# Optimization experiments

Hardware: AMD Instinct MI355X
Metric: run time of the kernel (lower is better)

## Reference

```python
import jax, jax.numpy as jnp
import numpy as np

NEG_SLOPE = 0.2


def setup_inputs() -> dict:
    key = jax.random.key(0)
    k1, k2, k3 = jax.random.split(key, 3)
    bs, n_agents, input_dim = 32, 512, 128
    n_heads, hidden_dim = 8, 64
    h = jax.random.normal(k1, (bs, n_agents, input_dim), dtype=jnp.float32)
    # Linear(input_dim, n_heads*hidden_dim, bias=False), stored as [in, out]
    W = jax.random.normal(k2, (input_dim, n_heads * hidden_dim), dtype=jnp.float32) * (1.0 / np.sqrt(input_dim))
    # xavier_uniform with gain=1.414 on shape (1, n_heads, 2*hidden_dim)
    fan = n_heads + 2 * hidden_dim
    bound = 1.414 * np.sqrt(6.0 / fan)
    att_a = jax.random.uniform(k3, (1, n_heads, 2 * hidden_dim), dtype=jnp.float32,
                               minval=-bound, maxval=bound)
    return {"h": h, "W": W, "att_a": att_a}


def reference(h, W, att_a):
    bs, n_agents, _ = h.shape
    n_heads = att_a.shape[1]
    hidden_dim = att_a.shape[2] // 2
    # h_prime: [bs, n_heads, n_agents, hidden_dim]
    h_prime = (h @ W).reshape(bs, n_agents, n_heads, hidden_dim).transpose(0, 2, 1, 3)
    # Additive score decomposes exactly: (a1.h_i + a2.h_j) == sum(cat(h_i,h_j)*a)
    a_src = att_a[0, :, :hidden_dim]   # [n_heads, hidden_dim]
    a_dst = att_a[0, :, hidden_dim:]   # [n_heads, hidden_dim]
    e_src = jnp.einsum('bhnd,hd->bhn', h_prime, a_src)  # score contribution of node i (row)
    e_dst = jnp.einsum('bhnd,hd->bhn', h_prime, a_dst)  # contribution of node j (col)
    e = e_src[:, :, :, None] + e_dst[:, :, None, :]     # [bs, n_heads, n, n]
    e = jnp.where(e >= 0, e, NEG_SLOPE * e)             # leaky_relu(0.2)
    attention = jax.nn.softmax(e, axis=-1)
    h_new = jnp.einsum('bhnm,bhmd->bhnd', attention, h_prime)
    return jax.nn.elu(h_new)
```

## Files before the change

kernel.cpp:

```cpp
#include <hip/hip_runtime.h>

#define BS 32
#define NA 512
#define ID 128
#define NH 8
#define HD 64
#define NHD 512
#define NEG 0.2f
#define BPAD 136
#define VSTR 520

typedef short bf16x8 __attribute__((ext_vector_type(8)));
typedef float f32x4 __attribute__((ext_vector_type(4)));
typedef int   i32x4 __attribute__((ext_vector_type(4)));

__device__ inline unsigned f2bf_bits(float x) {
  unsigned u = __float_as_uint(x);
  return (u + 0x7FFFu + ((u >> 16) & 1u)) >> 16;
}

__device__ inline void split8(const float4& x, const float4& y,
                              bf16x8& hi, bf16x8& lo) {
  float f[8] = {x.x, x.y, x.z, x.w, y.x, y.y, y.z, y.w};
  #pragma unroll
  for (int j = 0; j < 8; ++j) {
    unsigned hb = f2bf_bits(f[j]);
    float r = f[j] - __uint_as_float(hb << 16);
    unsigned lb = f2bf_bits(r);
    hi[j] = (short)hb;
    lo[j] = (short)lb;
  }
}

__global__ __launch_bounds__(256, 4) void k1_mfma(
    const float* __restrict__ h, const float* __restrict__ W,
    const float* __restrict__ att, float* __restrict__ hp,
    float* __restrict__ sG, float* __restrict__ tG) {
  __shared__ unsigned short Bhi[64 * BPAD];
  __shared__ unsigned short Blo[64 * BPAD];

  int blk = blockIdx.x;
  int mt = blk >> 3;
  int n0 = (blk & 7) * 64;
  int m0 = mt * 128;
  int b = mt >> 2;
  int nbase = (mt & 3) * 128;
  int head = n0 >> 6;
  int t = threadIdx.x;
  int lane = t & 63, w = t >> 6;
  int q = lane >> 4, ml = lane & 15;

  {
    int c = t & 63, kq = t >> 6;
    const float* wsrc = W + (size_t)kq * 32 * NHD + n0 + c;
    #pragma unroll 4
    for (int kk = 0; kk < 32; ++kk) {
      int k = kq * 32 + kk;
      float x = wsrc[(size_t)kk * NHD];
      unsigned hb = f2bf_bits(x);
      float r = x - __uint_as_float(hb << 16);
      Bhi[c * BPAD + k] = (unsigned short)hb;
      Blo[c * BPAD + k] = (unsigned short)f2bf_bits(r);
    }
  }
  __syncthreads();

  f32x4 acc[2][4];
  #pragma unroll
  for (int mf = 0; mf < 2; ++mf)
    #pragma unroll
    for (int nf = 0; nf < 4; ++nf)
      acc[mf][nf] = (f32x4){0.f, 0.f, 0.f, 0.f};

  const float* A0 = h + (size_t)(m0 + w * 32 + ml) * ID;

  #pragma unroll
  for (int ks = 0; ks < 4; ++ks) {
    int ko = ks * 32 + q * 8;
    bf16x8 ah[2], al[2];
    #pragma unroll
    for (int mf = 0; mf < 2; ++mf) {
      const float* ap = A0 + mf * 16 * ID + ko;
      float4 f0 = *(const float4*)ap;
      float4 f1 = *(const float4*)(ap + 4);
      split8(f0, f1, ah[mf], al[mf]);
    }
    #pragma unroll
    for (int nf = 0; nf < 4; ++nf) {
      int bo = (nf * 16 + ml) * BPAD + ko;
      bf16x8 bh = *(const bf16x8*)&Bhi[bo];
      bf16x8 bl = *(const bf16x8*)&Blo[bo];
      #pragma unroll
      for (int mf = 0; mf < 2; ++mf) {
        acc[mf][nf] = __builtin_amdgcn_mfma_f32_16x16x32_bf16(ah[mf], bh, acc[mf][nf], 0, 0, 0);
        acc[mf][nf] = __builtin_amdgcn_mfma_f32_16x16x32_bf16(ah[mf], bl, acc[mf][nf], 0, 0, 0);
        acc[mf][nf] = __builtin_amdgcn_mfma_f32_16x16x32_bf16(al[mf], bh, acc[mf][nf], 0, 0, 0);
      }
    }
  }

  {
    float* ob = hp + (((size_t)b * NH + head) * NA + nbase + w * 32) * HD + ml;
    #pragma unroll
    for (int mf = 0; mf < 2; ++mf)
      #pragma unroll
      for (int nf = 0; nf < 4; ++nf)
        #pragma unroll
        for (int r = 0; r < 4; ++r)
          ob[(size_t)(mf * 16 + q * 4 + r) * HD + nf * 16] = acc[mf][nf][r];
  }

  {
    float a_s[4], a_d[4];
    #pragma unroll
    for (int nf = 0; nf < 4; ++nf) {
      a_s[nf] = att[head * 128 + nf * 16 + ml];
      a_d[nf] = att[head * 128 + 64 + nf * 16 + ml];
    }
    #pragma unroll
    for (int mf = 0; mf < 2; ++mf) {
      #pragma unroll
      for (int r = 0; r < 4; ++r) {
        float sp = 0.f, tp = 0.f;
        #pragma unroll
        for (int nf = 0; nf < 4; ++nf) {
          float c = acc[mf][nf][r];
          sp += c * a_s[nf]; tp += c * a_d[nf];
        }
        #pragma unroll
        for (int m = 1; m < 16; m <<= 1) {
          sp += __shfl_xor(sp, m, 64);
          tp += __shfl_xor(tp, m, 64);
        }
        if (ml == 0) {
          int row = nbase + w * 32 + mf * 16 + q * 4 + r;
          size_t o = ((size_t)b * NH + head) * NA + row;
          sG[o] = sp; tG[o] = tp;
        }
      }
    }
  }
}

__global__ __launch_bounds__(512, 2) void k2_flash(
    const float* __restrict__ hp, const float* __restrict__ sG,
    const float* __restrict__ tG, float* __restrict__ out) {
  __shared__ unsigned short VTh[64 * VSTR];
  __shared__ unsigned short VTl[64 * VSTR];
  __shared__ float tS[NA]; __shared__ float sS[NA];
  __shared__ float sA[NA]; __shared__ float sB[NA];
  __shared__ float wpS[NA]; __shared__ float wnS[NA];
  __shared__ float wnVp[8 * 64]; __shared__ float wnV[64];
  __shared__ float red[8]; __shared__ float red2[8];

  int bh = blockIdx.x;
  int t = threadIdx.x;
  int lane = t & 63, w = t >> 6;
  int q = lane >> 4, ml = lane & 15;
  const float* vb = hp + (size_t)bh * NA * HD;

  float tj = tG[(size_t)bh * NA + t];
  float sj = sG[(size_t)bh * NA + t];
  tS[t] = tj; sS[t] = sj;
  {
    float m = tj;
    #pragma unroll
    for (int d = 32; d; d >>= 1) m = fmaxf(m, __shfl_xor(m, d, 64));
    if (lane == 0) red[w] = m;
  }
  __syncthreads();
  float tmax = fmaxf(fmaxf(fmaxf(red[0], red[1]), fmaxf(red[2], red[3])),
                     fmaxf(fmaxf(red[4], red[5]), fmaxf(red[6], red[7])));

  float wpj = __expf(tj - tmax);
  float wnj = __expf(0.2f * (tj - tmax));
  wpS[t] = wpj; wnS[t] = wnj;
  {
    float y = sj + tmax;
    float lr = fmaxf(y, 0.2f * y);
    sA[t] = __expf(y - lr);
    sB[t] = __expf(0.2f * y - lr);
  }
  {
    float ws = wnj;
    #pragma unroll
    for (int d = 32; d; d >>= 1) ws += __shfl_xor(ws, d, 64);
    if (lane == 0) red2[w] = ws;
  }
  __syncthreads();
  float wnSum = ((red2[0] + red2[1]) + (red2[2] + red2[3])) +
                ((red2[4] + red2[5]) + (red2[6] + red2[7]));

  {
    int d = lane;
    float part = 0.f;
    #pragma unroll 1
    for (int g = 0; g < 8; ++g) {
      int j0 = w * 64 + g * 8;
      unsigned hw0, hw1, hw2, hw3, lw0, lw1, lw2, lw3;
#define TRPAIR(KP, HW, LW)                                                    \
      { float v0 = vb[(size_t)(j0 + 2*(KP)) * HD + d];                        \
        float v1 = vb[(size_t)(j0 + 2*(KP) + 1) * HD + d];                    \
        part += wnS[j0 + 2*(KP)] * v0 + wnS[j0 + 2*(KP) + 1] * v1;            \
        unsigned h0 = f2bf_bits(v0), h1 = f2bf_bits(v1);                      \
        unsigned l0 = f2bf_bits(v0 - __uint_as_float(h0 << 16));              \
        unsigned l1 = f2bf_bits(v1 - __uint_as_float(h1 << 16));              \
        HW = h0 | (h1 << 16); LW = l0 | (l1 << 16); }
      TRPAIR(0, hw0, lw0) TRPAIR(1, hw1, lw1)
      TRPAIR(2, hw2, lw2) TRPAIR(3, hw3, lw3)
#undef TRPAIR
      uint4 hv = {hw0, hw1, hw2, hw3};
      uint4 lv = {lw0, lw1, lw2, lw3};
      *(uint4*)&VTh[d * VSTR + j0] = hv;
      *(uint4*)&VTl[d * VSTR + j0] = lv;
    }
    wnVp[w * 64 + d] = part;
  }
  __syncthreads();
  if (t < 64) {
    float a = 0.f;
    #pragma unroll
    for (int ww = 0; ww < 8; ++ww) a += wnVp[ww * 64 + t];
    wnV[t] = a;
  }
  __syncthreads();

  int ri = w * 64;
  float sIr[4], Ar[4], Br[4];
  #pragma unroll
  for (int mf = 0; mf < 4; ++mf) {
    int rr = ri + mf * 16 + ml;
    sIr[mf] = sS[rr]; Ar[mf] = sA[rr]; Br[mf] = sB[rr];
  }

  f32x4 acc[4][4], aD[4];
  #pragma unroll
  for (int mf = 0; mf < 4; ++mf) {
    #pragma unroll
    for (int nf = 0; nf < 4; ++nf) acc[mf][nf] = (f32x4){0.f, 0.f, 0.f, 0.f};
    aD[mf] = (f32x4){0.f, 0.f, 0.f, 0.f};
  }

  bf16x8 ONESB;
  {
    int ov = (ml == 0) ? (int)0x3F803F80 : 0;
    i32x4 o = {ov, ov, ov, ov};
    ONESB = __builtin_bit_cast(bf16x8, o);
  }

  #pragma unroll 1
  for (int ch = 0; ch < 16; ++ch) {
    int j0q = ch * 32 + q * 8;
    float4 wpa = *(const float4*)&wpS[j0q];
    float4 wpb = *(const float4*)&wpS[j0q + 4];
    float4 wna = *(const float4*)&wnS[j0q];
    float4 wnb = *(const float4*)&wnS[j0q + 4];
    float4 tqa = *(const float4*)&tS[j0q];
    float4 tqb = *(const float4*)&tS[j0q + 4];
    bf16x8 vh[4], vl[4];
    #pragma unroll
    for (int nf = 0; nf < 4; ++nf) {
      int dd = nf * 16 + ml;
      vh[nf] = *(const bf16x8*)&VTh[dd * VSTR + j0q];
      vl[nf] = *(const bf16x8*)&VTl[dd * VSTR + j0q];
    }
    #pragma unroll
    for (int mf = 0; mf < 4; ++mf) {
      float si = sIr[mf], A = Ar[mf], B = Br[mf];
      float c0 = (si + tqa.x >= 0.f) ? fmaf(A, wpa.x, -(B * wna.x)) : 0.f;
      float c1 = (si + tqa.y >= 0.f) ? fmaf(A, wpa.y, -(B * wna.y)) : 0.f;
      float c2 = (si + tqa.z >= 0.f) ? fmaf(A, wpa.z, -(B * wna.z)) : 0.f;
      float c3 = (si + tqa.w >= 0.f) ? fmaf(A, wpa.w, -(B * wna.w)) : 0.f;
      float c4 = (si + tqb.x >= 0.f) ? fmaf(A, wpb.x, -(B * wnb.x)) : 0.f;
      float c5 = (si + tqb.y >= 0.f) ? fmaf(A, wpb.y, -(B * wnb.y)) : 0.f;
      float c6 = (si + tqb.z >= 0.f) ? fmaf(A, wpb.z, -(B * wnb.z)) : 0.f;
      float c7 = (si + tqb.w >= 0.f) ? fmaf(A, wpb.w, -(B * wnb.w)) : 0.f;
      unsigned h0 = f2bf_bits(c0), h1 = f2bf_bits(c1), h2 = f2bf_bits(c2),
               h3 = f2bf_bits(c3), h4 = f2bf_bits(c4), h5 = f2bf_bits(c5),
               h6 = f2bf_bits(c6), h7 = f2bf_bits(c7);
      i32x4 uh = {(int)(h0 | (h1 << 16)), (int)(h2 | (h3 << 16)),
                  (int)(h4 | (h5 << 16)), (int)(h6 | (h7 << 16))};
      unsigned l0 = f2bf_bits(c0 - __uint_as_float(h0 << 16));
      unsigned l1 = f2bf_bits(c1 - __uint_as_float(h1 << 16));
      unsigned l2 = f2bf_bits(c2 - __uint_as_float(h2 << 16));
      unsigned l3 = f2bf_bits(c3 - __uint_as_float(h3 << 16));
      unsigned l4 = f2bf_bits(c4 - __uint_as_float(h4 << 16));
      unsigned l5 = f2bf_bits(c5 - __uint_as_float(h5 << 16));
      unsigned l6 = f2bf_bits(c6 - __uint_as_float(h6 << 16));
      unsigned l7 = f2bf_bits(c7 - __uint_as_float(h7 << 16));
      i32x4 ul = {(int)(l0 | (l1 << 16)), (int)(l2 | (l3 << 16)),
                  (int)(l4 | (l5 << 16)), (int)(l6 | (l7 << 16))};
      bf16x8 Ph = __builtin_bit_cast(bf16x8, uh);
      bf16x8 Pl = __builtin_bit_cast(bf16x8, ul);
      #pragma unroll
      for (int nf = 0; nf < 4; ++nf) {
        acc[mf][nf] = __builtin_amdgcn_mfma_f32_16x16x32_bf16(Ph, vh[nf], acc[mf][nf], 0, 0, 0);
        acc[mf][nf] = __builtin_amdgcn_mfma_f32_16x16x32_bf16(Pl, vh[nf], acc[mf][nf], 0, 0, 0);
        acc[mf][nf] = __builtin_amdgcn_mfma_f32_16x16x32_bf16(Ph, vl[nf], acc[mf][nf], 0, 0, 0);
      }
      aD[mf] = __builtin_amdgcn_mfma_f32_16x16x32_bf16(Ph, ONESB, aD[mf], 0, 0, 0);
      aD[mf] = __builtin_amdgcn_mfma_f32_16x16x32_bf16(Pl, ONESB, aD[mf], 0, 0, 0);
    }
  }

  {
    float* ob = out + (size_t)bh * NA * HD;
    #pragma unroll
    for (int mf = 0; mf < 4; ++mf) {
      #pragma unroll
      for (int r = 0; r < 4; ++r) {
        float dv = __shfl(aD[mf][r], lane & 48, 64);
        int row = ri + mf * 16 + q * 4 + r;
        float Brow = sB[row];
        float inv = 1.f / fmaf(Brow, wnSum, dv);
        #pragma unroll
        for (int nf = 0; nf < 4; ++nf) {
          int d = nf * 16 + ml;
          float x = fmaf(Brow, wnV[d], acc[mf][nf][r]) * inv;
          ob[(size_t)row * HD + d] = x > 0.f ? x : __expf(x) - 1.f;
        }
      }
    }
  }
}

extern "C" void kernel_launch(void* const* d_in, const int* in_sizes, int n_in,
                              void* d_out, int out_size, void* d_ws, size_t ws_size,
                              hipStream_t stream) {
  const float* h   = (const float*)d_in[0];
  const float* W   = (const float*)d_in[1];
  const float* att = (const float*)d_in[2];
  float* out = (float*)d_out;
  const size_t R = (size_t)BS * NH * NA;
  float* hp = (float*)d_ws;
  float* sG = hp + R * HD;
  float* tG = sG + R;

  k1_mfma <<<dim3(1024),    dim3(256), 0, stream>>>(h, W, att, hp, sG, tG);
  k2_flash<<<dim3(BS * NH), dim3(512), 0, stream>>>(hp, sG, tG, out);
}
```

Measured before the change: 132.3 us.

## Use 1024-thread blocks in flash kernel and switch to truncating bf16 split

Doubles the k2_flash block to 16 waves, each owning 32 query rows instead of 64, and halves the per-wave transpose loop. The inner loop is reordered so P fragments are built first and V fragments are loaded per nf, which lowers register pressure. The bf16 hi/lo split now truncates instead of rounding, saving ALU work but making the hi part less accurate (the lo term still carries the residual). With 256 blocks on the GPU, each block has more waves to hide latency, though each V fragment is now reused across fewer rows.

```diff
diff --git a/kernel.cpp b/kernel.cpp
--- a/kernel.cpp
+++ b/kernel.cpp
@@ -142,7 +142,17 @@
   }
 }
 
-__global__ __launch_bounds__(512, 2) void k2_flash(
+__device__ inline unsigned packpair_hi(float c0, float c1, float& r0, float& r1) {
+  unsigned u0 = __float_as_uint(c0), u1 = __float_as_uint(c1);
+  r0 = c0 - __uint_as_float(u0 & 0xFFFF0000u);
+  r1 = c1 - __uint_as_float(u1 & 0xFFFF0000u);
+  return (u0 >> 16) | (u1 & 0xFFFF0000u);
+}
+__device__ inline unsigned packpair_tr(float r0, float r1) {
+  return (__float_as_uint(r0) >> 16) | (__float_as_uint(r1) & 0xFFFF0000u);
+}
+
+__global__ __launch_bounds__(1024) void k2_flash(
     const float* __restrict__ hp, const float* __restrict__ sG,
     const float* __restrict__ tG, float* __restrict__ out) {
   __shared__ unsigned short VTh[64 * VSTR];
@@ -150,7 +160,7 @@
   __shared__ float tS[NA]; __shared__ float sS[NA];
   __shared__ float sA[NA]; __shared__ float sB[NA];
   __shared__ float wpS[NA]; __shared__ float wnS[NA];
-  __shared__ float wnVp[8 * 64]; __shared__ float wnV[64];
+  __shared__ float wnVp[16 * 64]; __shared__ float wnV[64];
   __shared__ float red[8]; __shared__ float red2[8];
 
   int bh = blockIdx.x;
@@ -159,10 +169,13 @@
   int q = lane >> 4, ml = lane & 15;
   const float* vb = hp + (size_t)bh * NA * HD;
 
-  float tj = tG[(size_t)bh * NA + t];
-  float sj = sG[(size_t)bh * NA + t];
-  tS[t] = tj; sS[t] = sj;
-  {
+  float tj = 0.f, sj = 0.f;
+  if (t < NA) {
+    tj = tG[(size_t)bh * NA + t];
+    sj = sG[(size_t)bh * NA + t];
+    tS[t] = tj; sS[t] = sj;
+  }
+  if (w < 8) {
     float m = tj;
     #pragma unroll
     for (int d = 32; d; d >>= 1) m = fmaxf(m, __shfl_xor(m, d, 64));
@@ -172,16 +185,17 @@
   float tmax = fmaxf(fmaxf(fmaxf(red[0], red[1]), fmaxf(red[2], red[3])),
                      fmaxf(fmaxf(red[4], red[5]), fmaxf(red[6], red[7])));
 
-  float wpj = __expf(tj - tmax);
-  float wnj = __expf(0.2f * (tj - tmax));
-  wpS[t] = wpj; wnS[t] = wnj;
-  {
+  float wnj = 0.f;
+  if (t < NA) {
+    float wpj = __expf(tj - tmax);
+    wnj = __expf(0.2f * (tj - tmax));
+    wpS[t] = wpj; wnS[t] = wnj;
     float y = sj + tmax;
     float lr = fmaxf(y, 0.2f * y);
     sA[t] = __expf(y - lr);
     sB[t] = __expf(0.2f * y - lr);
   }
-  {
+  if (w < 8) {
     float ws = wnj;
     #pragma unroll
     for (int d = 32; d; d >>= 1) ws += __shfl_xor(ws, d, 64);
@@ -195,17 +209,16 @@
     int d = lane;
     float part = 0.f;
     #pragma unroll 1
-    for (int g = 0; g < 8; ++g) {
-      int j0 = w * 64 + g * 8;
+    for (int g = 0; g < 4; ++g) {
+      int j0 = w * 32 + g * 8;
       unsigned hw0, hw1, hw2, hw3, lw0, lw1, lw2, lw3;
 #define TRPAIR(KP, HW, LW)                                                    \
       { float v0 = vb[(size_t)(j0 + 2*(KP)) * HD + d];                        \
         float v1 = vb[(size_t)(j0 + 2*(KP) + 1) * HD + d];                    \
         part += wnS[j0 + 2*(KP)] * v0 + wnS[j0 + 2*(KP) + 1] * v1;            \
-        unsigned h0 = f2bf_bits(v0), h1 = f2bf_bits(v1);                      \
-        unsigned l0 = f2bf_bits(v0 - __uint_as_float(h0 << 16));              \
-        unsigned l1 = f2bf_bits(v1 - __uint_as_float(h1 << 16));              \
-        HW = h0 | (h1 << 16); LW = l0 | (l1 << 16); }
+        float r0_, r1_;                                                       \
+        HW = packpair_hi(v0, v1, r0_, r1_);                                   \
+        LW = packpair_tr(r0_, r1_); }
       TRPAIR(0, hw0, lw0) TRPAIR(1, hw1, lw1)
       TRPAIR(2, hw2, lw2) TRPAIR(3, hw3, lw3)
 #undef TRPAIR
@@ -220,22 +233,22 @@
   if (t < 64) {
     float a = 0.f;
     #pragma unroll
-    for (int ww = 0; ww < 8; ++ww) a += wnVp[ww * 64 + t];
+    for (int ww = 0; ww < 16; ++ww) a += wnVp[ww * 64 + t];
     wnV[t] = a;
   }
   __syncthreads();
 
-  int ri = w * 64;
-  float sIr[4], Ar[4], Br[4];
-  #pragma unroll
-  for (int mf = 0; mf < 4; ++mf) {
+  int ri = w * 32;
+  float sIr[2], Ar[2], Br[2];
+  #pragma unroll
+  for (int mf = 0; mf < 2; ++mf) {
     int rr = ri + mf * 16 + ml;
     sIr[mf] = sS[rr]; Ar[mf] = sA[rr]; Br[mf] = sB[rr];
   }
 
-  f32x4 acc[4][4], aD[4];
-  #pragma unroll
-  for (int mf = 0; mf < 4; ++mf) {
+  f32x4 acc[2][4], aD[2];
+  #pragma unroll
+  for (int mf = 0; mf < 2; ++mf) {
     #pragma unroll
     for (int nf = 0; nf < 4; ++nf) acc[mf][nf] = (f32x4){0.f, 0.f, 0.f, 0.f};
     aD[mf] = (f32x4){0.f, 0.f, 0.f, 0.f};
@@ -257,15 +270,9 @@
     float4 wnb = *(const float4*)&wnS[j0q + 4];
     float4 tqa = *(const float4*)&tS[j0q];
     float4 tqb = *(const float4*)&tS[j0q + 4];
-    bf16x8 vh[4], vl[4];
-    #pragma unroll
-    for (int nf = 0; nf < 4; ++nf) {
-      int dd = nf * 16 + ml;
-      vh[nf] = *(const bf16x8*)&VTh[dd * VSTR + j0q];
-      vl[nf] = *(const bf16x8*)&VTl[dd * VSTR + j0q];
-    }
-    #pragma unroll
-    for (int mf = 0; mf < 4; ++mf) {
+    bf16x8 Ph[2], Pl[2];
+    #pragma unroll
+    for (int mf = 0; mf < 2; ++mf) {
       float si = sIr[mf], A = Ar[mf], B = Br[mf];
       float c0 = (si + tqa.x >= 0.f) ? fmaf(A, wpa.x, -(B * wna.x)) : 0.f;
       float c1 = (si + tqa.y >= 0.f) ? fmaf(A, wpa.y, -(B * wna.y)) : 0.f;
@@ -275,38 +282,39 @@
       float c5 = (si + tqb.y >= 0.f) ? fmaf(A, wpb.y, -(B * wnb.y)) : 0.f;
       float c6 = (si + tqb.z >= 0.f) ? fmaf(A, wpb.z, -(B * wnb.z)) : 0.f;
       float c7 = (si + tqb.w >= 0.f) ? fmaf(A, wpb.w, -(B * wnb.w)) : 0.f;
-      unsigned h0 = f2bf_bits(c0), h1 = f2bf_bits(c1), h2 = f2bf_bits(c2),
-               h3 = f2bf_bits(c3), h4 = f2bf_bits(c4), h5 = f2bf_bits(c5),
-               h6 = f2bf_bits(c6), h7 = f2bf_bits(c7);
-      i32x4 uh = {(int)(h0 | (h1 << 16)), (int)(h2 | (h3 << 16)),
-                  (int)(h4 | (h5 << 16)), (int)(h6 | (h7 << 16))};
-      unsigned l0 = f2bf_bits(c0 - __uint_as_float(h0 << 16));
-      unsigned l1 = f2bf_bits(c1 - __uint_as_float(h1 << 16));
-      unsigned l2 = f2bf_bits(c2 - __uint_as_float(h2 << 16));
-      unsigned l3 = f2bf_bits(c3 - __uint_as_float(h3 << 16));
-      unsigned l4 = f2bf_bits(c4 - __uint_as_float(h4 << 16));
-      unsigned l5 = f2bf_bits(c5 - __uint_as_float(h5 << 16));
-      unsigned l6 = f2bf_bits(c6 - __uint_as_float(h6 << 16));
-      unsigned l7 = f2bf_bits(c7 - __uint_as_float(h7 << 16));
-      i32x4 ul = {(int)(l0 | (l1 << 16)), (int)(l2 | (l3 << 16)),
-                  (int)(l4 | (l5 << 16)), (int)(l6 | (l7 << 16))};
-      bf16x8 Ph = __builtin_bit_cast(bf16x8, uh);
-      bf16x8 Pl = __builtin_bit_cast(bf16x8, ul);
-      #pragma unroll
-      for (int nf = 0; nf < 4; ++nf) {
-        acc[mf][nf] = __builtin_amdgcn_mfma_f32_16x16x32_bf16(Ph, vh[nf], acc[mf][nf], 0, 0, 0);
-        acc[mf][nf] = __builtin_amdgcn_mfma_f32_16x16x32_bf16(Pl, vh[nf], acc[mf][nf], 0, 0, 0);
-        acc[mf][nf] = __builtin_amdgcn_mfma_f32_16x16x32_bf16(Ph, vl[nf], acc[mf][nf], 0, 0, 0);
+      float r0, r1, r2, r3, r4, r5, r6, r7;
+      i32x4 uh = {(int)packpair_hi(c0, c1, r0, r1),
+                  (int)packpair_hi(c2, c3, r2, r3),
+                  (int)packpair_hi(c4, c5, r4, r5),
+                  (int)packpair_hi(c6, c7, r6, r7)};
+      i32x4 ul = {(int)packpair_tr(r0, r1), (int)packpair_tr(r2, r3),
+                  (int)packpair_tr(r4, r5), (int)packpair_tr(r6, r7)};
+      Ph[mf] = __builtin_bit_cast(bf16x8, uh);
+      Pl[mf] = __builtin_bit_cast(bf16x8, ul);
+    }
+    #pragma unroll
+    for (int nf = 0; nf < 4; ++nf) {
+      int dd = nf * 16 + ml;
+      bf16x8 vh = *(const bf16x8*)&VTh[dd * VSTR + j0q];
+      bf16x8 vl = *(const bf16x8*)&VTl[dd * VSTR + j0q];
+      #pragma unroll
+      for (int mf = 0; mf < 2; ++mf) {
+        acc[mf][nf] = __builtin_amdgcn_mfma_f32_16x16x32_bf16(Ph[mf], vh, acc[mf][nf], 0, 0, 0);
+        acc[mf][nf] = __builtin_amdgcn_mfma_f32_16x16x32_bf16(Pl[mf], vh, acc[mf][nf], 0, 0, 0);
+        acc[mf][nf] = __builtin_amdgcn_mfma_f32_16x16x32_bf16(Ph[mf], vl, acc[mf][nf], 0, 0, 0);
       }
-      aD[mf] = __builtin_amdgcn_mfma_f32_16x16x32_bf16(Ph, ONESB, aD[mf], 0, 0, 0);
-      aD[mf] = __builtin_amdgcn_mfma_f32_16x16x32_bf16(Pl, ONESB, aD[mf], 0, 0, 0);
+    }
+    #pragma unroll
+    for (int mf = 0; mf < 2; ++mf) {
+      aD[mf] = __builtin_amdgcn_mfma_f32_16x16x32_bf16(Ph[mf], ONESB, aD[mf], 0, 0, 0);
+      aD[mf] = __builtin_amdgcn_mfma_f32_16x16x32_bf16(Pl[mf], ONESB, aD[mf], 0, 0, 0);
     }
   }
 
   {
     float* ob = out + (size_t)bh * NA * HD;
     #pragma unroll
-    for (int mf = 0; mf < 4; ++mf) {
+    for (int mf = 0; mf < 2; ++mf) {
       #pragma unroll
       for (int r = 0; r < 4; ++r) {
         float dv = __shfl(aD[mf][r], lane & 48, 64);
@@ -336,6 +344,6 @@
   float* sG = hp + R * HD;
   float* tG = sG + R;
 
-  k1_mfma <<<dim3(1024),    dim3(256), 0, stream>>>(h, W, att, hp, sG, tG);
-  k2_flash<<<dim3(BS * NH), dim3(512), 0, stream>>>(hp, sG, tG, out);
-}
+  k1_mfma <<<dim3(1024),     dim3(256),  0, stream>>>(h, W, att, hp, sG, tG);
+  k2_flash<<<dim3(BS * NH), dim3(1024), 0, stream>>>(hp, sG, tG, out);
+}
```

Result: faster. 126.9 us (-4.1%).
